# Optimization experiments

Measured on AMD Instinct MI355X. Metric: run time of the kernel, lower is better.

Reference implementation:

```python
import jax, jax.numpy as jnp
import numpy as np

EPS = 1e-5
B, C, H, W = 128, 512, 32, 32


def setup_inputs() -> dict:
    key = jax.random.key(0)
    ks = jax.random.split(key, 3)
    s = 1.0 / np.sqrt(C)
    return {
        "x": jax.random.normal(ks[0], (B, C, H, W), dtype=jnp.float32),
        "ln_w": jnp.ones((C, H, W), dtype=jnp.float32),
        "ln_b": jnp.zeros((C, H, W), dtype=jnp.float32),
        "w1": jax.random.uniform(ks[1], (C, C), dtype=jnp.float32, minval=-s, maxval=s),
        "b1": jnp.zeros((C,), dtype=jnp.float32),
        "w2": jax.random.uniform(ks[2], (C, C), dtype=jnp.float32, minval=-s, maxval=s),
        "b2": jnp.zeros((C,), dtype=jnp.float32),
    }


def reference(x, ln_w, ln_b, w1, b1, w2, b2):
    b, c, h, w = x.shape
    # LayerNorm over the full (C, H, W) feature volume per sample
    mu = jnp.mean(x, axis=(1, 2, 3), keepdims=True)
    var = jnp.mean(jnp.square(x - mu), axis=(1, 2, 3), keepdims=True)
    xn = (x - mu) * jax.lax.rsqrt(var + EPS) * ln_w + ln_b
    # tokens: (B, H*W, C)
    t = xn.reshape(b, c, h * w).transpose(0, 2, 1)
    hdn = jax.nn.relu(jnp.einsum('bsc,dc->bsd', t, w1) + b1)
    out = jnp.einsum('bsd,ed->bse', hdn, w2) + b2
    return out.transpose(0, 2, 1).reshape(b, c, h, w)
```

## Files before the change

kernel.cpp:

```cpp
#include <hip/hip_runtime.h>
#include <stdint.h>


#define NSAMP 128
#define CCH   512
#define HWSZ  1024
#define NPER  (CCH*HWSZ)

typedef unsigned short u16;
typedef __bf16 bf16x8 __attribute__((ext_vector_type(8)));
typedef float  f32x4  __attribute__((ext_vector_type(4)));

__device__ __forceinline__ float b2f(u16 h){ return __uint_as_float(((unsigned)h)<<16); }
__device__ __forceinline__ u16 f2b(float f){
  unsigned u = __float_as_uint(f);
  u += 0x7FFFu + ((u>>16)&1u);
  return (u16)(u>>16);
}
__device__ __forceinline__ void unpack8(uint4 v, float* f){
  const unsigned* u = (const unsigned*)&v;
#pragma unroll
  for (int q=0;q<4;q++){
    f[2*q]   = __uint_as_float(u[q]<<16);
    f[2*q+1] = __uint_as_float(u[q]&0xFFFF0000u);
  }
}
__device__ __forceinline__ void load8(const void* base, size_t idx, int isf, float* f){
  if (isf){
    const float* p = (const float*)base + idx;
    uint4 a = *(const uint4*)p;
    uint4 b = *(const uint4*)(p+4);
    const float* af = (const float*)&a;
    const float* bf = (const float*)&b;
#pragma unroll
    for (int j=0;j<4;j++){ f[j]=af[j]; f[4+j]=bf[j]; }
  } else {
    uint4 v = *(const uint4*)((const u16*)base + idx);
    unpack8(v, f);
  }
}
__device__ __forceinline__ void store8b(u16* dst, const float* f){
  uint4 o; unsigned* ou = (unsigned*)&o;
#pragma unroll
  for (int q=0;q<4;q++) ou[q] = (unsigned)f2b(f[2*q]) | ((unsigned)f2b(f[2*q+1])<<16);
  *(uint4*)dst = o;
}

__device__ __forceinline__ void gload_lds16(const u16* g, u16* l){
  __builtin_amdgcn_global_load_lds(
      (const __attribute__((address_space(1))) void*)g,
      (__attribute__((address_space(3))) void*)l,
      16, 0, 0);
}

__global__ __launch_bounds__(256) void detect_kernel(const u16* __restrict__ x,
                                                     int* __restrict__ flag){
  __shared__ int sh[256];
  int tid = threadIdx.x, cnt = 0;
  for (int i=tid; i<16384; i+=256){
    unsigned e = ((unsigned)x[i] >> 7) & 0xFFu;
    cnt += (e >= 0xC0u);
  }
  sh[tid] = cnt; __syncthreads();
  for (int s=128; s; s>>=1){ if (tid<s) sh[tid]+=sh[tid+s]; __syncthreads(); }
  if (tid==0) flag[0] = sh[0];
}

__global__ __launch_bounds__(256) void convert_kernel(
    const void* __restrict__ w1, const void* __restrict__ w2,
    const void* __restrict__ b1, const void* __restrict__ b2,
    const void* __restrict__ lw, const void* __restrict__ lb,
    const int* __restrict__ flag,
    u16* __restrict__ w1b, u16* __restrict__ w2b,
    float* __restrict__ b1f, float* __restrict__ b2f,
    u16* __restrict__ lwb, u16* __restrict__ lbb){
  int isf = flag[0] > 64;
  int t = blockIdx.x*256 + threadIdx.x;
  size_t i8 = (size_t)t*8;
  float f[8];
  if (t < 32768){
    load8(w1, i8, isf, f); store8b(w1b + i8, f);
    load8(w2, i8, isf, f); store8b(w2b + i8, f);
  }
  load8(lw, i8, isf, f); store8b(lwb + i8, f);
  load8(lb, i8, isf, f); store8b(lbb + i8, f);
  if (t < 64){
    load8(b1, i8, isf, f);
#pragma unroll
    for (int j=0;j<8;j++) b1f[i8+j] = f[j];
    load8(b2, i8, isf, f);
#pragma unroll
    for (int j=0;j<8;j++) b2f[i8+j] = f[j];
  }
}

__global__ __launch_bounds__(256) void stats_kernel(const void* __restrict__ x,
                                                    float* __restrict__ stats,
                                                    const int* __restrict__ flag){
  int isf = flag[0] > 64;
  int b   = blockIdx.y;
  int blk = blockIdx.x;
  size_t base = (size_t)b*NPER + (size_t)blk*32768;
  int tid = threadIdx.x;
  float s1 = 0.f, s2 = 0.f;
#pragma unroll
  for (int i=0;i<16;i++){
    float f[8];
    load8(x, base + i*2048 + tid*8, isf, f);
#pragma unroll
    for (int j=0;j<8;j++){ s1 += f[j]; s2 += f[j]*f[j]; }
  }
#pragma unroll
  for (int off=32; off; off>>=1){
    s1 += __shfl_down(s1, off);
    s2 += __shfl_down(s2, off);
  }
  __shared__ float r1[4], r2[4];
  int w = tid>>6, lane = tid&63;
  if (lane==0){ r1[w]=s1; r2[w]=s2; }
  __syncthreads();
  if (tid==0){
    atomicAdd(&stats[2*b],   r1[0]+r1[1]+r1[2]+r1[3]);
    atomicAdd(&stats[2*b+1], r2[0]+r2[1]+r2[2]+r2[3]);
  }
}

__global__ __launch_bounds__(256) void lnT_kernel(const void* __restrict__ x,
                                                  const u16* __restrict__ lwb,
                                                  const u16* __restrict__ lbb,
                                                  const float* __restrict__ stats,
                                                  const int* __restrict__ flag,
                                                  int gb0,
                                                  u16* __restrict__ xnT){
  int isf = flag[0] > 64;
  int bl = blockIdx.z;
  int gb = gb0 + bl;
  int c0 = blockIdx.y*64;
  int s0 = blockIdx.x*64;
  const float invN = 1.f/(float)NPER;
  float mu  = stats[2*gb]*invN;
  float var = fmaxf(stats[2*gb+1]*invN - mu*mu, 0.f);
  float rs  = rsqrtf(var + 1e-5f);

  __shared__ float T[64][65];
  int tid = threadIdx.x;
  int tr  = tid>>3;
  int tcl = (tid&7)*8;

#pragma unroll
  for (int p=0;p<2;p++){
    int c = c0 + p*32 + tr;
    size_t idx = (size_t)c*HWSZ + s0 + tcl;
    float xf[8], wf[8], bf_[8];
    load8(x, (size_t)gb*NPER + idx, isf, xf);
    unpack8(*(const uint4*)(lwb + idx), wf);
    unpack8(*(const uint4*)(lbb + idx), bf_);
    float* dst = &T[p*32 + tr][tcl];
#pragma unroll
    for (int j=0;j<8;j++) dst[j] = (xf[j]-mu)*rs*wf[j] + bf_[j];
  }
  __syncthreads();
#pragma unroll
  for (int p=0;p<2;p++){
    int srow = p*32 + tr;
    float tmp[8];
#pragma unroll
    for (int j=0;j<8;j++) tmp[j] = T[tcl+j][srow];
    store8b(xnT + ((size_t)bl*HWSZ + s0 + srow)*CCH + c0 + tcl, tmp);
  }
}

template<int RELU, int BIASM, int MFIRST, int NOUT, int DUALOUT>
__global__ __launch_bounds__(256) void gemm_kernel(
    const u16* __restrict__ A, long sA,
    const u16* __restrict__ B, long sB,
    const float* __restrict__ bias,
    u16* __restrict__ Co,
    const int* __restrict__ flag, int gb0)
{
  __shared__ __align__(16) u16 sh[32768];

  int b  = blockIdx.y;
  int bx = blockIdx.x;
  int tm, tn;
  if (MFIRST){ tm = bx & 7; tn = bx >> 3; }
  else       { tn = bx & 7; tm = bx >> 3; }
  const u16* Ab = A + (size_t)b*sA + (size_t)(tm*128)*512;
  const u16* Bb = B + (size_t)b*sB + (size_t)(tn*128)*512;

  int tid  = threadIdx.x;
  int lane = tid & 63;
  int w    = tid >> 6;
  int wm   = w >> 1, wn = w & 1;
  int l15  = lane & 15;
  int q    = lane >> 4;
  int sw   = l15 & 7;

  int ar  = tid >> 3;
  int acs = ((tid & 7) ^ (ar & 7)) * 8;
  const u16* aSrc = Ab + (size_t)ar*512 + acs;
  const u16* bSrc = Bb + (size_t)ar*512 + acs;

  f32x4 acc[4][4];
#pragma unroll
  for (int i=0;i<4;i++)
#pragma unroll
    for (int j=0;j<4;j++) acc[i][j] = (f32x4){0.f,0.f,0.f,0.f};

  auto STAGE = [&](int p, int kk){
    u16* aD = sh + p*16384 + tid*8;
    u16* bD = sh + p*16384 + 8192 + tid*8;
#pragma unroll
    for (int j=0;j<4;j++) gload_lds16(aSrc + j*16384 + kk, aD + j*2048);
#pragma unroll
    for (int j=0;j<4;j++) gload_lds16(bSrc + j*16384 + kk, bD + j*2048);
  };
  auto COMPUTE = [&](int p){
    const u16* Asb = sh + p*16384;
    const u16* Bsb = sh + p*16384 + 8192;
#pragma unroll
    for (int ks=0; ks<2; ks++){
      bf16x8 fa[4], fb[4];
      int pc = ((ks*4 + q) ^ sw) * 8;
#pragma unroll
      for (int i=0;i<4;i++){
        fa[i] = *(const bf16x8*)(Asb + (wm*64 + i*16 + l15)*64 + pc);
        fb[i] = *(const bf16x8*)(Bsb + (wn*64 + i*16 + l15)*64 + pc);
      }
#pragma unroll
      for (int i=0;i<4;i++)
#pragma unroll
        for (int jn=0;jn<4;jn++)
          acc[i][jn] = __builtin_amdgcn_mfma_f32_16x16x32_bf16(fa[i], fb[jn], acc[i][jn], 0,0,0);
    }
  };

  STAGE(0, 0);
#pragma unroll
  for (int t=0; t<7; t++){
    STAGE((t+1)&1, (t+1)*64);
    asm volatile("s_waitcnt vmcnt(8)" ::: "memory");
    __builtin_amdgcn_s_barrier();
    __builtin_amdgcn_sched_barrier(0);
    COMPUTE(t & 1);
    __builtin_amdgcn_s_barrier();
  }
  asm volatile("s_waitcnt vmcnt(0)" ::: "memory");
  __builtin_amdgcn_s_barrier();
  __builtin_amdgcn_sched_barrier(0);
  COMPUTE(1);
  __syncthreads();

  int isf = DUALOUT ? (flag[0] > 64) : 0;
  size_t sampOff = (size_t)(gb0 + b) * NPER;
  int row0 = tm*128, col0 = tn*128;

  if (!DUALOUT || !isf){
    u16* Cb = Co + sampOff;
#pragma unroll
    for (int i=0;i<4;i++){
#pragma unroll
      for (int jn=0;jn<4;jn++){
        int n = wn*64 + jn*16 + l15;
        float bn = BIASM ? 0.f : bias[col0 + n];
#pragma unroll
        for (int r=0;r<4;r++){
          int m = wm*64 + i*16 + q*4 + r;
          float v = acc[i][jn][r] + (BIASM ? bias[row0 + m] : bn);
          if (RELU) v = fmaxf(v, 0.f);
          sh[m*128 + (n ^ ((m&7)<<3))] = f2b(v);
        }
      }
    }
    __syncthreads();
    int rr  = tid >> 1;
    int c0_ = (tid & 1)*8;
#pragma unroll
    for (int j=0;j<8;j++){
      int c = c0_ + j;
      uint4 vv = *(const uint4*)(sh + rr*128 + ((c ^ (rr&7))<<3));
      *(uint4*)(Cb + (size_t)(row0+rr)*NOUT + col0 + (c<<3)) = vv;
    }
  } else {
    float* Cf  = (float*)Co + sampOff;
    float* shf = (float*)sh;
#pragma unroll
    for (int i=0;i<4;i++){
#pragma unroll
      for (int jn=0;jn<4;jn++){
        int n = wn*64 + jn*16 + l15;
        float bn = BIASM ? 0.f : bias[col0 + n];
#pragma unroll
        for (int r=0;r<4;r++){
          int m = wm*64 + i*16 + q*4 + r;
          float v = acc[i][jn][r] + (BIASM ? bias[row0 + m] : bn);
          if (RELU) v = fmaxf(v, 0.f);
          shf[m*128 + (((n>>2) ^ (m&7))<<2) + (n&3)] = v;
        }
      }
    }
    __syncthreads();
    int rr = tid >> 1;
    int hf = (tid & 1)*16;
#pragma unroll
    for (int j=0;j<16;j++){
      int c = hf + j;
      uint4 vv = *(const uint4*)(shf + rr*128 + ((c ^ (rr&7))<<2));
      *(uint4*)(Cf + (size_t)(row0+rr)*NOUT + col0 + (c<<2)) = vv;
    }
  }
}

extern "C" void kernel_launch(void* const* d_in, const int* in_sizes, int n_in,
                              void* d_out, int out_size, void* d_ws, size_t ws_size,
                              hipStream_t stream) {
  (void)in_sizes; (void)n_in; (void)out_size;
  const void* x  = d_in[0];
  const void* lw = d_in[1];
  const void* lb = d_in[2];
  const void* w1 = d_in[3];
  const void* b1 = d_in[4];
  const void* w2 = d_in[5];
  const void* b2 = d_in[6];

  char* ws = (char*)d_ws;
  float* stats = (float*)ws;
  int*   flag  = (int*)(ws + 1024);
  float* b1f   = (float*)(ws + 2048);
  float* b2f   = (float*)(ws + 4096);
  u16*   w1b   = (u16*)(ws + 8192);
  u16*   w2b   = (u16*)(ws + 8192 + 524288);
  u16*   lwb   = (u16*)(ws + 1179648);
  u16*   lbb   = (u16*)(ws + 1179648 + 1048576);
  u16*   xnT   = (u16*)(ws + (size_t)(4u<<20));

  long gmax = ((long)ws_size - (4L<<20)) / (2L<<20);
  int G = (int)(gmax < 1 ? 1 : (gmax > 128 ? 128 : gmax));
  u16* hdnT = xnT + (size_t)G*NPER;

  hipMemsetAsync(d_ws, 0, 2048, stream);
  detect_kernel<<<1,256,0,stream>>>((const u16*)x, flag);
  convert_kernel<<<256,256,0,stream>>>(w1, w2, b1, b2, lw, lb, flag,
                                       w1b, w2b, b1f, b2f, lwb, lbb);
  stats_kernel<<<dim3(16,NSAMP),256,0,stream>>>(x, stats, flag);

  for (int b0=0; b0<NSAMP; b0+=G){
    int Gi = (NSAMP-b0 < G) ? (NSAMP-b0) : G;
    lnT_kernel<<<dim3(HWSZ/64, CCH/64, Gi),256,0,stream>>>(x, lwb, lbb, stats, flag, b0, xnT);
    gemm_kernel<1,0,1,512,0><<<dim3(32,Gi),256,0,stream>>>(
        xnT, (long)NPER, w1b, 0L, b1f, hdnT, flag, 0);
    gemm_kernel<0,1,0,1024,1><<<dim3(32,Gi),256,0,stream>>>(
        w2b, 0L, hdnT, (long)NPER, b2f, (u16*)d_out, flag, b0);
  }
}
```

Measured before the change: 783.5 us.

## Enlarge GEMM tiles to 256x256 with 512-thread blocks

Grows the GEMM block tile from 128x128 to 256x256 using 8 waves, each wave computing a 128x64 sub-tile, with shared memory doubled to 128 KB for double-buffered stages. The aim is more reuse of each loaded A/B tile and less global and LDS traffic per MFMA. The fp32 epilogue now writes out in two half-tile passes to fit in shared memory. The risks are fewer blocks (8 per sample instead of 32), which can leave CUs idle when the sample group is small, and higher register pressure from 32 accumulators per lane that may force a single block per CU.

```diff
diff --git a/kernel.cpp b/kernel.cpp
--- a/kernel.cpp
+++ b/kernel.cpp
@@ -171,27 +171,30 @@
 }
 
 template<int RELU, int BIASM, int MFIRST, int NOUT, int DUALOUT>
-__global__ __launch_bounds__(256) void gemm_kernel(
+__global__ __launch_bounds__(512, 2) void gemm_kernel(
     const u16* __restrict__ A, long sA,
     const u16* __restrict__ B, long sB,
     const float* __restrict__ bias,
     u16* __restrict__ Co,
     const int* __restrict__ flag, int gb0)
 {
-  __shared__ __align__(16) u16 sh[32768];
+  __shared__ __align__(16) u16 sh[65536];
+
+  constexpr int NTN = NOUT/256;
+  constexpr int NTM = 8/NTN;
 
   int b  = blockIdx.y;
   int bx = blockIdx.x;
   int tm, tn;
-  if (MFIRST){ tm = bx & 7; tn = bx >> 3; }
-  else       { tn = bx & 7; tm = bx >> 3; }
-  const u16* Ab = A + (size_t)b*sA + (size_t)(tm*128)*512;
-  const u16* Bb = B + (size_t)b*sB + (size_t)(tn*128)*512;
+  if (MFIRST){ tm = bx % NTM; tn = bx / NTM; }
+  else       { tn = bx % NTN; tm = bx / NTN; }
+  const u16* Ab = A + (size_t)b*sA + (size_t)(tm*256)*512;
+  const u16* Bb = B + (size_t)b*sB + (size_t)(tn*256)*512;
 
   int tid  = threadIdx.x;
   int lane = tid & 63;
   int w    = tid >> 6;
-  int wm   = w >> 1, wn = w & 1;
+  int wm   = w >> 2, wn = w & 3;
   int l15  = lane & 15;
   int q    = lane >> 4;
   int sw   = l15 & 7;
@@ -201,34 +204,35 @@
   const u16* aSrc = Ab + (size_t)ar*512 + acs;
   const u16* bSrc = Bb + (size_t)ar*512 + acs;
 
-  f32x4 acc[4][4];
-#pragma unroll
-  for (int i=0;i<4;i++)
+  f32x4 acc[8][4];
+#pragma unroll
+  for (int i=0;i<8;i++)
 #pragma unroll
     for (int j=0;j<4;j++) acc[i][j] = (f32x4){0.f,0.f,0.f,0.f};
 
   auto STAGE = [&](int p, int kk){
-    u16* aD = sh + p*16384 + tid*8;
-    u16* bD = sh + p*16384 + 8192 + tid*8;
-#pragma unroll
-    for (int j=0;j<4;j++) gload_lds16(aSrc + j*16384 + kk, aD + j*2048);
-#pragma unroll
-    for (int j=0;j<4;j++) gload_lds16(bSrc + j*16384 + kk, bD + j*2048);
+    u16* aD = sh + p*32768 + tid*8;
+    u16* bD = sh + p*32768 + 16384 + tid*8;
+#pragma unroll
+    for (int j=0;j<4;j++) gload_lds16(aSrc + (size_t)j*32768 + kk, aD + j*4096);
+#pragma unroll
+    for (int j=0;j<4;j++) gload_lds16(bSrc + (size_t)j*32768 + kk, bD + j*4096);
   };
   auto COMPUTE = [&](int p){
-    const u16* Asb = sh + p*16384;
-    const u16* Bsb = sh + p*16384 + 8192;
+    const u16* Asb = sh + p*32768;
+    const u16* Bsb = Asb + 16384;
 #pragma unroll
     for (int ks=0; ks<2; ks++){
-      bf16x8 fa[4], fb[4];
+      bf16x8 fa[8], fb[4];
       int pc = ((ks*4 + q) ^ sw) * 8;
 #pragma unroll
-      for (int i=0;i<4;i++){
-        fa[i] = *(const bf16x8*)(Asb + (wm*64 + i*16 + l15)*64 + pc);
-        fb[i] = *(const bf16x8*)(Bsb + (wn*64 + i*16 + l15)*64 + pc);
-      }
-#pragma unroll
-      for (int i=0;i<4;i++)
+      for (int i=0;i<8;i++)
+        fa[i] = *(const bf16x8*)(Asb + (wm*128 + i*16 + l15)*64 + pc);
+#pragma unroll
+      for (int jn=0;jn<4;jn++)
+        fb[jn] = *(const bf16x8*)(Bsb + (wn*64 + jn*16 + l15)*64 + pc);
+#pragma unroll
+      for (int i=0;i<8;i++)
 #pragma unroll
         for (int jn=0;jn<4;jn++)
           acc[i][jn] = __builtin_amdgcn_mfma_f32_16x16x32_bf16(fa[i], fb[jn], acc[i][jn], 0,0,0);
@@ -253,49 +257,22 @@
 
   int isf = DUALOUT ? (flag[0] > 64) : 0;
   size_t sampOff = (size_t)(gb0 + b) * NPER;
-  int row0 = tm*128, col0 = tn*128;
+  int row0 = tm*256, col0 = tn*256;
 
   if (!DUALOUT || !isf){
     u16* Cb = Co + sampOff;
 #pragma unroll
-    for (int i=0;i<4;i++){
+    for (int i=0;i<8;i++){
 #pragma unroll
       for (int jn=0;jn<4;jn++){
         int n = wn*64 + jn*16 + l15;
         float bn = BIASM ? 0.f : bias[col0 + n];
 #pragma unroll
         for (int r=0;r<4;r++){
-          int m = wm*64 + i*16 + q*4 + r;
+          int m = wm*128 + i*16 + q*4 + r;
           float v = acc[i][jn][r] + (BIASM ? bias[row0 + m] : bn);
           if (RELU) v = fmaxf(v, 0.f);
-          sh[m*128 + (n ^ ((m&7)<<3))] = f2b(v);
-        }
-      }
-    }
-    __syncthreads();
-    int rr  = tid >> 1;
-    int c0_ = (tid & 1)*8;
-#pragma unroll
-    for (int j=0;j<8;j++){
-      int c = c0_ + j;
-      uint4 vv = *(const uint4*)(sh + rr*128 + ((c ^ (rr&7))<<3));
-      *(uint4*)(Cb + (size_t)(row0+rr)*NOUT + col0 + (c<<3)) = vv;
-    }
-  } else {
-    float* Cf  = (float*)Co + sampOff;
-    float* shf = (float*)sh;
-#pragma unroll
-    for (int i=0;i<4;i++){
-#pragma unroll
-      for (int jn=0;jn<4;jn++){
-        int n = wn*64 + jn*16 + l15;
-        float bn = BIASM ? 0.f : bias[col0 + n];
-#pragma unroll
-        for (int r=0;r<4;r++){
-          int m = wm*64 + i*16 + q*4 + r;
-          float v = acc[i][jn][r] + (BIASM ? bias[row0 + m] : bn);
-          if (RELU) v = fmaxf(v, 0.f);
-          shf[m*128 + (((n>>2) ^ (m&7))<<2) + (n&3)] = v;
+          sh[m*256 + (((n>>3) ^ (m&7))<<3) + (n&7)] = f2b(v);
         }
       }
     }
@@ -305,8 +282,40 @@
 #pragma unroll
     for (int j=0;j<16;j++){
       int c = hf + j;
-      uint4 vv = *(const uint4*)(shf + rr*128 + ((c ^ (rr&7))<<2));
-      *(uint4*)(Cf + (size_t)(row0+rr)*NOUT + col0 + (c<<2)) = vv;
+      uint4 vv = *(const uint4*)(sh + rr*256 + ((c ^ (rr&7))<<3));
+      *(uint4*)(Cb + (size_t)(row0+rr)*NOUT + col0 + (c<<3)) = vv;
+    }
+  } else {
+    float* Cf  = (float*)Co + sampOff;
+    float* shf = (float*)sh;
+#pragma unroll
+    for (int p=0;p<2;p++){
+      if (p) __syncthreads();
+      if (wm == p){
+#pragma unroll
+        for (int i=0;i<8;i++){
+#pragma unroll
+          for (int jn=0;jn<4;jn++){
+            int n = wn*64 + jn*16 + l15;
+            float bn = BIASM ? 0.f : bias[col0 + n];
+#pragma unroll
+            for (int r=0;r<4;r++){
+              int ml = i*16 + q*4 + r;
+              float v = acc[i][jn][r] + (BIASM ? bias[row0 + p*128 + ml] : bn);
+              if (RELU) v = fmaxf(v, 0.f);
+              shf[ml*256 + (((n>>2) ^ (ml&7))<<2) + (n&3)] = v;
+            }
+          }
+        }
+      }
+      __syncthreads();
+      int rr = tid >> 2, qt = tid & 3;
+#pragma unroll
+      for (int j=0;j<16;j++){
+        int c = qt*16 + j;
+        uint4 vv = *(const uint4*)(shf + rr*256 + ((c ^ (rr&7))<<2));
+        *(uint4*)(Cf + (size_t)(row0 + p*128 + rr)*NOUT + col0 + (c<<2)) = vv;
+      }
     }
   }
 }
@@ -347,9 +356,9 @@
   for (int b0=0; b0<NSAMP; b0+=G){
     int Gi = (NSAMP-b0 < G) ? (NSAMP-b0) : G;
     lnT_kernel<<<dim3(HWSZ/64, CCH/64, Gi),256,0,stream>>>(x, lwb, lbb, stats, flag, b0, xnT);
-    gemm_kernel<1,0,1,512,0><<<dim3(32,Gi),256,0,stream>>>(
+    gemm_kernel<1,0,1,512,0><<<dim3(8,Gi),512,0,stream>>>(
         xnT, (long)NPER, w1b, 0L, b1f, hdnT, flag, 0);
-    gemm_kernel<0,1,0,1024,1><<<dim3(32,Gi),256,0,stream>>>(
+    gemm_kernel<0,1,0,1024,1><<<dim3(8,Gi),512,0,stream>>>(
         w2b, 0L, hdnT, (long)NPER, b2f, (u16*)d_out, flag, b0);
   }
 }
```

Result: slower. 876.2 us (+11.8%).
